# Optimization experiments

Hardware: AMD Instinct MI355X
Metric: run time of the kernel (lower is better)

The kernel has to match this reference:

```python
import jax, jax.numpy as jnp
import numpy as np
from jax import lax

B, N, T, D_IN, D_OUT, LINK_LEN, EMBED = 32, 500, 12, 1, 64, 3, 10
C_WIN = 1            # x_window feature dim ((dim_in-1)%16==0 branch)
CNN_CH = D_OUT // 16  # 4 channels per topology CNN


def setup_inputs() -> dict:
    key = jax.random.key(0)
    ks = jax.random.split(key, 16)
    s = 0.1
    inp = {}
    inp["x"] = jax.random.normal(ks[0], (B, N, D_IN), jnp.float32)
    inp["x_window"] = jax.random.normal(ks[1], (B, T, N, C_WIN), jnp.float32)
    inp["node_embeddings"] = jax.random.normal(ks[2], (N, EMBED), jnp.float32)
    inp["adj"] = jax.random.uniform(ks[3], (N, N), jnp.float32)
    inp["MPG"] = jax.random.normal(ks[4], (B, T, N, N), jnp.float32)
    inp["bootstrap_idx"] = jnp.sort(jax.random.randint(ks[5], (3,), 0, T))
    inp["fixed_adj"] = 0
    inp["stay_cost"] = 1
    inp["jump_cost"] = 2
    inp["weights_pool"] = jax.random.normal(ks[6], (EMBED, LINK_LEN, D_IN, 3 * D_OUT // 4), jnp.float32) * s
    inp["window_weights_supra"] = jax.random.normal(ks[7], (EMBED, C_WIN, D_OUT // 8), jnp.float32) * s
    inp["window_weights_temporal"] = jax.random.normal(ks[8], (EMBED, C_WIN, D_OUT // 8), jnp.float32) * s
    inp["bias_pool"] = jax.random.normal(ks[9], (EMBED, D_OUT), jnp.float32) * s
    inp["T_param"] = jax.random.normal(ks[10], (T,), jnp.float32) * s
    inp["conv_mean_w"] = jax.random.normal(ks[11], (CNN_CH, T, 3, 3), jnp.float32) * s
    inp["conv_mean_b"] = jnp.zeros((CNN_CH,), jnp.float32)
    inp["conv_max_w"] = jax.random.normal(ks[12], (CNN_CH, T, 3, 3), jnp.float32) * s
    inp["conv_max_b"] = jnp.zeros((CNN_CH,), jnp.float32)
    return inp


def _conv2d(x, w, b):
    y = lax.conv_general_dilated(x, w, (1, 1), 'SAME',
                                 dimension_numbers=('NCHW', 'OIHW', 'NCHW'))
    return y + b[None, :, None, None]


def reference(x, x_window, node_embeddings, adj, MPG, bootstrap_idx, fixed_adj,
              stay_cost, jump_cost, weights_pool, window_weights_supra,
              window_weights_temporal, bias_pool, T_param,
              conv_mean_w, conv_mean_b, conv_max_w, conv_max_b):
    n = node_embeddings.shape[0]
    eye = jnp.eye(n, dtype=x.dtype)
    # adaptive adjacency from node embeddings, diagonal set to stay_cost
    s0 = jax.nn.relu(node_embeddings @ node_embeddings.T)
    s0 = jnp.where(eye > 0, jnp.asarray(stay_cost, x.dtype), s0)
    if fixed_adj == 1:
        S = adj * jnp.exp(s0)
    else:
        S = jax.nn.softmax(s0, axis=1)
    # faithful to torch broadcast: S[i,j] / sum_k S[j,k]
    S = S / jnp.sum(S, axis=1)
    # multi-hop supports: I, S, S@S, ...
    supports = [eye, S]
    for k in range(2, LINK_LEN):
        supports.append(S @ supports[-1])
    supports = jnp.stack(supports, axis=0)  # [K, N, N]
    # supra-laplacian: diagonal blocks S, strictly-upper blocks jump_cost*I
    F_b = bootstrap_idx.shape[0]  # 3 bootstrap layers
    supra = (jnp.kron(jnp.eye(F_b, dtype=x.dtype), S)
             + jnp.kron(jnp.triu(jnp.ones((F_b, F_b), x.dtype), 1),
                        jnp.asarray(jump_cost, x.dtype) * eye))
    # node-adaptive weights/bias
    weights = jnp.einsum('nd,dkio->nkio', node_embeddings, weights_pool)
    bias = node_embeddings @ bias_pool  # [N, D_OUT]
    # spatial graph conv
    x_s = jnp.einsum('knm,bmc->bnkc', supports, x)
    x_sconv = jnp.einsum('bnki,nkio->bno', x_s, weights)  # [B,N,48]
    # supra-laplacian window conv over bootstrap slices
    ww_s = jnp.einsum('nd,dio->nio', node_embeddings, window_weights_supra)
    xw = x_window[:, bootstrap_idx]            # [B, 3, N, c]
    b_sz = xw.shape[0]
    xw_flat = xw.reshape(b_sz, F_b * n, -1)    # [B, 3N, c]
    xws = jnp.einsum('bmi,mn->bni', xw_flat, supra).reshape(b_sz, F_b, n, -1)
    x_wconv_s = jnp.einsum('bfni,nio->bfno', xws, ww_s).mean(axis=1)  # [B,N,8]
    # temporal window conv
    ww_t = jnp.einsum('nd,dio->nio', node_embeddings, window_weights_temporal)
    x_wconv_t = jnp.einsum('btni,nio,t->bno', x_window, ww_t, T_param)  # [B,N,8]
    # topology CNNs (conv + relu + global mean / max pool)
    topo_mean = jax.nn.relu(_conv2d(MPG, conv_mean_w, conv_mean_b)).mean(axis=(2, 3))
    topo_max = jax.nn.relu(_conv2d(MPG, conv_max_w, conv_max_b)).max(axis=(2, 3))
    topo = jnp.concatenate([topo_mean, topo_max], axis=1)  # [B, 8]
    x_twconv_s = x_wconv_s * topo[:, None, :]
    return jnp.concatenate([x_sconv, x_twconv_s, x_wconv_t], axis=-1) + bias[None]
```

## Files before the change

kernel.cpp:

```cpp
#include <hip/hip_runtime.h>

#define NN 500
#define BB 32
#define TT 12
#define EMB 10

typedef short bf16x8 __attribute__((ext_vector_type(8)));
typedef float f32x16 __attribute__((ext_vector_type(16)));

__device__ __forceinline__ unsigned short f2bf(float x) {
    unsigned int u = __float_as_uint(x);
    u = (u + 0x7fffu + ((u >> 16) & 1u)) >> 16;
    return (unsigned short)u;
}

__global__ __launch_bounds__(256) void k_softmaxS(const float* __restrict__ E,
                                                  const int* __restrict__ stay,
                                                  float* __restrict__ S) {
    const int i = blockIdx.x;
    const int tid = threadIdx.x;
    __shared__ float row[NN];
    __shared__ float red[256];
    float ei[EMB];
#pragma unroll
    for (int d = 0; d < EMB; ++d) ei[d] = E[i * EMB + d];
    const float stayf = (float)stay[0];

    float lmax = -1e30f;
    for (int j = tid; j < NN; j += 256) {
        float acc = 0.f;
#pragma unroll
        for (int d = 0; d < EMB; ++d) acc += ei[d] * E[j * EMB + d];
        float v = acc > 0.f ? acc : 0.f;
        if (j == i) v = stayf;
        row[j] = v;
        lmax = fmaxf(lmax, v);
    }
    red[tid] = lmax;
    __syncthreads();
    for (int s = 128; s > 0; s >>= 1) {
        if (tid < s) red[tid] = fmaxf(red[tid], red[tid + s]);
        __syncthreads();
    }
    const float rmax = red[0];
    __syncthreads();

    float lsum = 0.f;
    for (int j = tid; j < NN; j += 256) {
        float e = __expf(row[j] - rmax);
        row[j] = e;
        lsum += e;
    }
    red[tid] = lsum;
    __syncthreads();
    for (int s = 128; s > 0; s >>= 1) {
        if (tid < s) red[tid] += red[tid + s];
        __syncthreads();
    }
    const float inv = 1.0f / red[0];
    for (int j = tid; j < NN; j += 256) S[i * NN + j] = row[j] * inv;
}

__global__ __launch_bounds__(256) void k_matvecS(const float* __restrict__ S,
                                                 const float* __restrict__ xin,
                                                 float* __restrict__ yout) {
    const int b = blockIdx.y;
    const int w = threadIdx.x >> 6;
    const int lane = threadIdx.x & 63;
    const int n = blockIdx.x * 4 + w;
    const float* xb = xin + b * NN;
    const float* Sr = S + n * NN;
    float acc = 0.f;
    for (int m = lane; m < NN; m += 64) acc += Sr[m] * xb[m];
#pragma unroll
    for (int off = 32; off > 0; off >>= 1) acc += __shfl_down(acc, off, 64);
    if (lane == 0) yout[b * NN + n] = acc;
}

__global__ __launch_bounds__(256) void k_smallpre(const float* __restrict__ E,
                                                  const float* __restrict__ wp,
                                                  const float* __restrict__ bp,
                                                  const float* __restrict__ wwsp,
                                                  const float* __restrict__ wwtp,
                                                  float* __restrict__ W,
                                                  float* __restrict__ biasN,
                                                  float* __restrict__ wws,
                                                  float* __restrict__ wwt) {
    const int n = blockIdx.x;
    const int tid = threadIdx.x;
    __shared__ float e[EMB];
    if (tid < EMB) e[tid] = E[n * EMB + tid];
    __syncthreads();
    if (tid < 144) {
        float acc = 0.f;
#pragma unroll
        for (int d = 0; d < EMB; ++d) acc += e[d] * wp[d * 144 + tid];
        W[n * 144 + tid] = acc;
    } else if (tid < 208) {
        const int o = tid - 144;
        float acc = 0.f;
#pragma unroll
        for (int d = 0; d < EMB; ++d) acc += e[d] * bp[d * 64 + o];
        biasN[n * 64 + o] = acc;
    } else if (tid < 216) {
        const int o = tid - 208;
        float acc = 0.f;
#pragma unroll
        for (int d = 0; d < EMB; ++d) acc += e[d] * wwsp[d * 8 + o];
        wws[n * 8 + o] = acc;
    } else if (tid < 224) {
        const int o = tid - 216;
        float acc = 0.f;
#pragma unroll
        for (int d = 0; d < EMB; ++d) acc += e[d] * wwtp[d * 8 + o];
        wwt[n * 8 + o] = acc;
    }
}

__global__ __launch_bounds__(128) void k_Mwsum(const float* __restrict__ xwin,
                                               const float* __restrict__ S,
                                               const int* __restrict__ bidx,
                                               const int* __restrict__ jumpc,
                                               const float* __restrict__ Tp,
                                               float* __restrict__ M,
                                               float* __restrict__ wsum) {
    const int b = blockIdx.y;
    const int n0 = blockIdx.x * 125;
    const int tid = threadIdx.x;
    __shared__ float xsf[NN];
    __shared__ float Tl[TT];
    const int t0 = bidx[0], t1 = bidx[1], t2 = bidx[2];
    if (tid < TT) Tl[tid] = Tp[tid];
    const float* xb = xwin + (size_t)b * TT * NN;
    for (int m = tid; m < NN; m += 128)
        xsf[m] = xb[t0 * NN + m] + xb[t1 * NN + m] + xb[t2 * NN + m];
    __syncthreads();
    if (tid < 125) {
        const int n = n0 + tid;
        float ws_ = 0.f;
#pragma unroll
        for (int t = 0; t < TT; ++t) ws_ += xb[t * NN + n] * Tl[t];
        const float jc = (float)jumpc[0];
        const float jterm = jc * (2.f * xb[t0 * NN + n] + xb[t1 * NN + n]);
        float acc = 0.f;
        for (int m = 0; m < NN; ++m) acc += xsf[m] * S[m * NN + n];
        M[b * NN + n] = (acc + jterm) * (1.f / 3.f);
        wsum[b * NN + n] = ws_;
    }
}

__global__ __launch_bounds__(256) void k_wpackB(const float* __restrict__ wm,
                                                const float* __restrict__ wx,
                                                unsigned short* __restrict__ wq) {
    const int i = blockIdx.x * 256 + threadIdx.x;
    if (i >= 9 * 64 * 8) return;
    const int j = i & 7;
    const int rest = i >> 3;
    const int lane = rest & 63;
    const int s = rest >> 6;
    const int kh = s / 3, kw = s - kh * 3;
    const int n = lane & 31;
    const int t = (lane >> 5) * 8 + j;
    float v = 0.f;
    if (t < TT) {
        if (n < 4) v = wm[((n * TT + t) * 3 + kh) * 3 + kw];
        else if (n < 8) v = wx[(((n - 4) * TT + t) * 3 + kh) * 3 + kw];
    }
    wq[i] = f2bf(v);
}

#define SLOTW 132
#define SLOTS (SLOTW * 24)

__global__ __launch_bounds__(256, 2) void k_conv(const float* __restrict__ MPG,
                                                 const unsigned short* __restrict__ wq,
                                                 const float* __restrict__ bmv,
                                                 const float* __restrict__ bxv,
                                                 float* __restrict__ partials) {
    const int b = blockIdx.y;
    const int cb = blockIdx.x >> 3;
    const int rb = blockIdx.x & 7;
    const int C0 = cb * 128;
    const int R0 = rb * 63;
    const int R1 = (R0 + 62 < NN - 1) ? R0 + 62 : NN - 1;
    const int tid = threadIdx.x;
    const int w = __builtin_amdgcn_readfirstlane(tid >> 6);
    const int lane = tid & 63;
    const int hi = lane >> 5;

    __shared__ unsigned short lsd[4 * SLOTS];
    __shared__ float wred[4][8][2];

    const float* basef = MPG + (size_t)b * TT * NN * NN;

    bf16x8 bfq[9];
#pragma unroll
    for (int s = 0; s < 9; ++s)
        bfq[s] = *reinterpret_cast<const bf16x8*>(wq + (s * 64 + lane) * 8);

    int loff[7];
    size_t goff[7];
    bool okf[7], okc[7];
#pragma unroll
    for (int k = 0; k < 7; ++k) {
        const int f = tid + k * 256;
        okf[k] = (f < TT * SLOTW);
        const int t = f / SLOTW;
        const int sc = f - t * SLOTW;
        const int gcol = C0 - 1 + sc;
        okc[k] = okf[k] && (gcol >= 0) && (gcol < NN);
        goff[k] = (size_t)t * (NN * NN) + (okc[k] ? gcol : 0);
        loff[k] = sc * 24 + t;
    }

    for (int z = tid; z < 4 * SLOTW * 4; z += 256) {
        const int s = z / (SLOTW * 4);
        const int r2 = z - s * (SLOTW * 4);
        const int sc = r2 >> 2;
        lsd[s * SLOTS + sc * 24 + 12 + (r2 & 3)] = 0;
    }

    const int ch = lane & 31;
    const float biasv = (ch < 4) ? bmv[ch] : ((ch < 8) ? bxv[ch - 4] : 0.f);
    float mkv[16];
#pragma unroll
    for (int i = 0; i < 16; ++i) {
        const int p = C0 + w * 32 + (i & 3) + 8 * (i >> 2) + 4 * hi;
        mkv[i] = (p < NN) ? 1.f : 0.f;
    }
    const int aoff = (w * 32 + (lane & 31)) * 48 + hi * 16;

#pragma unroll
    for (int q = 0; q < 3; ++q) {
        const int rr = R0 - 1 + q;
        const bool rowok = (rr >= 0);
        float sv[7];
#pragma unroll
        for (int k = 0; k < 7; ++k)
            sv[k] = (rowok && okc[k]) ? basef[goff[k] + (size_t)rr * NN] : 0.f;
        unsigned short* dst = lsd + ((rr + 1) & 3) * SLOTS;
#pragma unroll
        for (int k = 0; k < 7; ++k)
            if (okf[k]) dst[loff[k]] = f2bf(sv[k]);
    }
    __syncthreads();

    float sumv = 0.f, maxv = 0.f;

    for (int r = R0; r <= R1; ++r) {
        const int rr = r + 2;
        const bool do_stage = (rr <= R1 + 1);
        float sv[7];
        if (do_stage) {
            const bool rowok = (rr < NN);
#pragma unroll
            for (int k = 0; k < 7; ++k)
                sv[k] = (rowok && okc[k]) ? basef[goff[k] + (size_t)rr * NN] : 0.f;
        }

        f32x16 acc;
#pragma unroll
        for (int i = 0; i < 16; ++i) acc[i] = biasv;
#pragma unroll
        for (int kh = 0; kh < 3; ++kh) {
            const char* sb = reinterpret_cast<const char*>(lsd + ((r + kh) & 3) * SLOTS);
#pragma unroll
            for (int kw = 0; kw < 3; ++kw) {
                const bf16x8 a = *reinterpret_cast<const bf16x8*>(sb + aoff + kw * 48);
                acc = __builtin_amdgcn_mfma_f32_32x32x16_bf16(a, bfq[kh * 3 + kw], acc, 0, 0, 0);
            }
        }
#pragma unroll
        for (int i = 0; i < 16; ++i) {
            const float v = fmaxf(acc[i], 0.f) * mkv[i];
            sumv += v;
            maxv = fmaxf(maxv, v);
        }

        if (do_stage) {
            unsigned short* dst = lsd + ((rr + 1) & 3) * SLOTS;
#pragma unroll
            for (int k = 0; k < 7; ++k)
                if (okf[k]) dst[loff[k]] = f2bf(sv[k]);
        }
        __syncthreads();
    }

    sumv += __shfl_xor(sumv, 32, 64);
    maxv = fmaxf(maxv, __shfl_xor(maxv, 32, 64));
    if (lane < 8) {
        wred[w][lane][0] = sumv;
        wred[w][lane][1] = maxv;
    }
    __syncthreads();
    if (tid < 8) {
        const float s = wred[0][tid][0] + wred[1][tid][0] + wred[2][tid][0] + wred[3][tid][0];
        const float mx = fmaxf(fmaxf(wred[0][tid][1], wred[1][tid][1]),
                               fmaxf(wred[2][tid][1], wred[3][tid][1]));
        partials[((size_t)b * 32 + blockIdx.x) * 8 + tid] = (tid < 4) ? s : mx;
    }
}

__global__ __launch_bounds__(256) void k_topo(const float* __restrict__ partials,
                                              float* __restrict__ topo) {
    const int b = blockIdx.x;
    const int tid = threadIdx.x;
    const int c = tid & 7;
    const int g = tid >> 3;
    float vs = 0.f, vm = 0.f;
    if (g < 32) {
        const float v = partials[((size_t)b * 32 + g) * 8 + c];
        vs = v;
        vm = v;
    }
    __shared__ float red[256];
    red[tid] = (c < 4) ? vs : vm;
    __syncthreads();
    for (int s = 16; s > 0; s >>= 1) {
        if (g < s) {
            const float a = red[tid];
            const float bv = red[tid + s * 8];
            red[tid] = (c < 4) ? (a + bv) : fmaxf(a, bv);
        }
        __syncthreads();
    }
    if (tid < 8) topo[b * 8 + tid] = (tid < 4) ? red[tid] * (1.f / (NN * (float)NN)) : red[tid];
}

__global__ __launch_bounds__(64) void k_out(const float* __restrict__ x,
                                            const float* __restrict__ y1,
                                            const float* __restrict__ y2,
                                            const float* __restrict__ W,
                                            const float* __restrict__ biasN,
                                            const float* __restrict__ wws,
                                            const float* __restrict__ wwt,
                                            const float* __restrict__ M,
                                            const float* __restrict__ wsum,
                                            const float* __restrict__ topo,
                                            float* __restrict__ out) {
    const int bn = blockIdx.x;
    const int b = bn / NN;
    const int n = bn - b * NN;
    const int o = threadIdx.x;
    float val;
    if (o < 48) {
        val = x[bn] * W[n * 144 + o] + y1[bn] * W[n * 144 + 48 + o] + y2[bn] * W[n * 144 + 96 + o];
    } else if (o < 56) {
        const int oo = o - 48;
        val = M[bn] * wws[n * 8 + oo] * topo[b * 8 + oo];
    } else {
        const int oo = o - 56;
        val = wsum[bn] * wwt[n * 8 + oo];
    }
    out[(size_t)bn * 64 + o] = val + biasN[n * 64 + o];
}

extern "C" void kernel_launch(void* const* d_in, const int* in_sizes, int n_in,
                              void* d_out, int out_size, void* d_ws, size_t ws_size,
                              hipStream_t stream) {
    const float* x    = (const float*)d_in[0];
    const float* xw   = (const float*)d_in[1];
    const float* E    = (const float*)d_in[2];
    const float* MPG  = (const float*)d_in[4];
    const int*   bidx = (const int*)d_in[5];
    const int*   stay = (const int*)d_in[7];
    const int*   jump = (const int*)d_in[8];
    const float* wp   = (const float*)d_in[9];
    const float* wwsp = (const float*)d_in[10];
    const float* wwtp = (const float*)d_in[11];
    const float* bp   = (const float*)d_in[12];
    const float* Tp   = (const float*)d_in[13];
    const float* cmw  = (const float*)d_in[14];
    const float* cmb  = (const float*)d_in[15];
    const float* cxw  = (const float*)d_in[16];
    const float* cxb  = (const float*)d_in[17];
    float* out = (float*)d_out;

    float* w = (float*)d_ws;
    float* S     = w;
    float* y1    = S + 250000;
    float* y2    = y1 + 16000;
    float* W     = y2 + 16000;
    float* biasN = W + 72000;
    float* wws   = biasN + 32000;
    float* wwt   = wws + 4000;
    float* M     = wwt + 4000;
    float* wsum  = M + 16000;
    float* parts = wsum + 16000;
    float* topo  = parts + 8192;
    float* wpckf = topo + 256;
    unsigned short* wq = (unsigned short*)wpckf;

    k_wpackB<<<18, 256, 0, stream>>>(cmw, cxw, wq);
    k_softmaxS<<<NN, 256, 0, stream>>>(E, stay, S);
    k_matvecS<<<dim3(125, BB), 256, 0, stream>>>(S, x, y1);
    k_matvecS<<<dim3(125, BB), 256, 0, stream>>>(S, y1, y2);
    k_smallpre<<<NN, 256, 0, stream>>>(E, wp, bp, wwsp, wwtp, W, biasN, wws, wwt);
    k_Mwsum<<<dim3(4, BB), 128, 0, stream>>>(xw, S, bidx, jump, Tp, M, wsum);
    k_conv<<<dim3(32, BB), 256, 0, stream>>>(MPG, wq, cmb, cxb, parts);
    k_topo<<<BB, 256, 0, stream>>>(parts, topo);
    k_out<<<BB * NN, 64, 0, stream>>>(x, y1, y2, W, biasN, wws, wwt, M, wsum, topo, out);
}
```

Before: 151.4 us.

## Reuse LDS row fragments across conv rows with rotating register buffers

The conv loop now keeps the A-fragments of the previous two input rows in registers and rotates three buffers, so each row step reads only one new row's fragments from LDS instead of three. The last row block is shifted to start at NN-63 and overlapping rows are masked out of the sums, giving every block a fixed 63-iteration loop that is manually unrolled by three. Launch bounds are raised to 3 blocks per SM to allow more occupancy, and the pad-zeroing loop uses 8-byte stores. The extra fragment registers may conflict with the tighter register budget that the higher occupancy target imposes.

After: 234.3 us. +54.8%, slower.

```diff
diff --git a/kernel.cpp b/kernel.cpp
--- a/kernel.cpp
+++ b/kernel.cpp
@@ -172,7 +172,7 @@
 #define SLOTW 132
 #define SLOTS (SLOTW * 24)
 
-__global__ __launch_bounds__(256, 2) void k_conv(const float* __restrict__ MPG,
+__global__ __launch_bounds__(256, 3) void k_conv(const float* __restrict__ MPG,
                                                  const unsigned short* __restrict__ wq,
                                                  const float* __restrict__ bmv,
                                                  const float* __restrict__ bxv,
@@ -181,8 +181,8 @@
     const int cb = blockIdx.x >> 3;
     const int rb = blockIdx.x & 7;
     const int C0 = cb * 128;
-    const int R0 = rb * 63;
-    const int R1 = (R0 + 62 < NN - 1) ? R0 + 62 : NN - 1;
+    const int rmin = rb * 63;
+    const int R0 = (rb < 7) ? rb * 63 : (NN - 63);
     const int tid = threadIdx.x;
     const int w = __builtin_amdgcn_readfirstlane(tid >> 6);
     const int lane = tid & 63;
@@ -213,11 +213,10 @@
         loff[k] = sc * 24 + t;
     }
 
-    for (int z = tid; z < 4 * SLOTW * 4; z += 256) {
-        const int s = z / (SLOTW * 4);
-        const int r2 = z - s * (SLOTW * 4);
-        const int sc = r2 >> 2;
-        lsd[s * SLOTS + sc * 24 + 12 + (r2 & 3)] = 0;
+    for (int z = tid; z < 4 * SLOTW; z += 256) {
+        const int s = z / SLOTW;
+        const int sc = z - s * SLOTW;
+        *reinterpret_cast<uint2*>(&lsd[s * SLOTS + sc * 24 + 12]) = uint2{0u, 0u};
     }
 
     const int ch = lane & 31;
@@ -246,44 +245,60 @@
     __syncthreads();
 
     float sumv = 0.f, maxv = 0.f;
-
-    for (int r = R0; r <= R1; ++r) {
+    bf16x8 fA[3], fB[3], fC[3];
+
+    auto FRAGRD = [&](bf16x8 (&F)[3], int row) {
+        const char* sb = reinterpret_cast<const char*>(lsd + ((row + 1) & 3) * SLOTS);
+#pragma unroll
+        for (int kw = 0; kw < 3; ++kw)
+            F[kw] = *reinterpret_cast<const bf16x8*>(sb + aoff + kw * 48);
+    };
+
+    auto STEP = [&](bf16x8 (&FX)[3], bf16x8 (&FY)[3], bf16x8 (&FZ)[3], const int r) {
         const int rr = r + 2;
-        const bool do_stage = (rr <= R1 + 1);
+        const bool rowok = (rr < NN);
         float sv[7];
-        if (do_stage) {
-            const bool rowok = (rr < NN);
-#pragma unroll
-            for (int k = 0; k < 7; ++k)
-                sv[k] = (rowok && okc[k]) ? basef[goff[k] + (size_t)rr * NN] : 0.f;
-        }
-
+#pragma unroll
+        for (int k = 0; k < 7; ++k)
+            sv[k] = (rowok && okc[k]) ? basef[goff[k] + (size_t)rr * NN] : 0.f;
+        FRAGRD(FZ, r + 1);
         f32x16 acc;
 #pragma unroll
         for (int i = 0; i < 16; ++i) acc[i] = biasv;
 #pragma unroll
-        for (int kh = 0; kh < 3; ++kh) {
-            const char* sb = reinterpret_cast<const char*>(lsd + ((r + kh) & 3) * SLOTS);
-#pragma unroll
-            for (int kw = 0; kw < 3; ++kw) {
-                const bf16x8 a = *reinterpret_cast<const bf16x8*>(sb + aoff + kw * 48);
-                acc = __builtin_amdgcn_mfma_f32_32x32x16_bf16(a, bfq[kh * 3 + kw], acc, 0, 0, 0);
-            }
-        }
+        for (int kw = 0; kw < 3; ++kw)
+            acc = __builtin_amdgcn_mfma_f32_32x32x16_bf16(FX[kw], bfq[kw], acc, 0, 0, 0);
+#pragma unroll
+        for (int kw = 0; kw < 3; ++kw)
+            acc = __builtin_amdgcn_mfma_f32_32x32x16_bf16(FY[kw], bfq[3 + kw], acc, 0, 0, 0);
+#pragma unroll
+        for (int kw = 0; kw < 3; ++kw)
+            acc = __builtin_amdgcn_mfma_f32_32x32x16_bf16(FZ[kw], bfq[6 + kw], acc, 0, 0, 0);
+        const float rm = (r >= rmin) ? 1.f : 0.f;
+        float rs = 0.f, rx = 0.f;
 #pragma unroll
         for (int i = 0; i < 16; ++i) {
             const float v = fmaxf(acc[i], 0.f) * mkv[i];
-            sumv += v;
-            maxv = fmaxf(maxv, v);
+            rs += v;
+            rx = fmaxf(rx, v);
         }
-
-        if (do_stage) {
-            unsigned short* dst = lsd + ((rr + 1) & 3) * SLOTS;
-#pragma unroll
-            for (int k = 0; k < 7; ++k)
-                if (okf[k]) dst[loff[k]] = f2bf(sv[k]);
-        }
+        sumv += rm * rs;
+        maxv = fmaxf(maxv, rm * rx);
+        unsigned short* dst = lsd + ((rr + 1) & 3) * SLOTS;
+#pragma unroll
+        for (int k = 0; k < 7; ++k)
+            if (okf[k]) dst[loff[k]] = f2bf(sv[k]);
         __syncthreads();
+    };
+
+    FRAGRD(fA, R0 - 1);
+    FRAGRD(fB, R0);
+
+#pragma unroll 1
+    for (int i = 0; i < 63; i += 3) {
+        STEP(fA, fB, fC, R0 + i);
+        STEP(fB, fC, fA, R0 + i + 1);
+        STEP(fC, fA, fB, R0 + i + 2);
     }
 
     sumv += __shfl_xor(sumv, 32, 64);
```
